# Kernel optimization log

Hardware: AMD Instinct MI355X
Metric: run time of the kernel (lower is better)

The kernel has to match this reference:

```python
import jax, jax.numpy as jnp
import numpy as np

EPS = 1e-08
ORDINAL = 2.0

def setup_inputs() -> dict:
    key = jax.random.key(0)
    k1, k2, k3, k4, k5 = jax.random.split(key, 5)
    B, IN, OUT = 1024, 256, 1024
    inputs = jax.random.normal(k1, (B, IN), dtype=jnp.float32)
    weights = jax.random.normal(k2, (OUT, IN), dtype=jnp.float32) * (1.0 / np.sqrt(IN))
    biases = jax.random.normal(k3, (OUT,), dtype=jnp.float32) * (1.0 / np.sqrt(IN))
    centers = jax.random.normal(k4, (OUT, IN), dtype=jnp.float32) * 0.1
    # diag inv covars ~ U(3/(IN+0.5), 3/(IN-0.5)) per reset_parameters
    inv_covars = jax.random.uniform(k5, (OUT, IN), dtype=jnp.float32,
                                    minval=3.0 / (IN + 0.5), maxval=3.0 / (IN - 0.5))
    return {"inputs": inputs, "weights": weights, "biases": biases,
            "centers": centers, "inv_covars": inv_covars}

def reference(inputs, weights, biases, centers, inv_covars):
    # linear part: [B, OUT]
    l = inputs @ weights.T + biases
    # diag covar path (ordinal = 2.0, so the 1e-32 stabilizer is absent and
    # pow(c^2, 1/ordinal) == |c| after clamping):
    # g[b, z] = sum_i ( |x[b,i] - c[z,i]| * sqrt(clamp(ic[z,i])^2) )^2
    ic = jnp.minimum(inv_covars, 1.0 / EPS)
    scale = jnp.power(ic * ic, 1.0 / ORDINAL)  # [OUT, IN]
    diff = jnp.abs(inputs[:, None, :] - centers[None, :, :]) * scale[None, :, :]  # [B, OUT, IN]
    g = jnp.exp(-jnp.sum(jnp.power(diff, ORDINAL), axis=-1))  # [B, OUT]
    res = l * g
    return (res, g)
```

## Files before the change

### kernel.cpp

```cpp
#include <hip/hip_runtime.h>
#include <math.h>


typedef __attribute__((ext_vector_type(8))) short short8;
typedef __attribute__((ext_vector_type(4))) float floatx4;

#define BDIM   1024
#define INDIM  256
#define OUTDIM 1024
#define AK     512
#define WK     256
#define GK     512

__device__ __forceinline__ unsigned short f2bf(float f) {
    union { float f; unsigned u; } v; v.f = f;
    unsigned r = v.u + 0x7FFFu + ((v.u >> 16) & 1u);
    return (unsigned short)(r >> 16);
}

__global__ __launch_bounds__(256)
void fgn_prep(const float* __restrict__ X, const float* __restrict__ W,
              const float* __restrict__ C, const float* __restrict__ IC,
              unsigned short* __restrict__ Ap, unsigned short* __restrict__ Wb,
              unsigned short* __restrict__ Gw, float* __restrict__ Cz)
{
    const int bid = blockIdx.x;
    if (bid < 256) {
        const int f   = bid * 256 + threadIdx.x;
        const int row = f >> 6;
        const int kq  = (f & 63) << 2;
        float4 x = *(const float4*)&X[row * INDIM + kq];
        ushort4 a, b;
        a.x = f2bf(x.x);      a.y = f2bf(x.y);      a.z = f2bf(x.z);      a.w = f2bf(x.w);
        b.x = f2bf(x.x*x.x);  b.y = f2bf(x.y*x.y);  b.z = f2bf(x.z*x.z);  b.w = f2bf(x.w*x.w);
        *(ushort4*)&Ap[row * AK + kq]         = a;
        *(ushort4*)&Ap[row * AK + INDIM + kq] = b;
    } else {
        const int z    = (bid - 256) * 4 + (threadIdx.x >> 6);
        const int lane = threadIdx.x & 63;
        const int k    = lane << 2;
        float4 w  = *(const float4*)&W [z * INDIM + k];
        float4 c  = *(const float4*)&C [z * INDIM + k];
        float4 ic = *(const float4*)&IC[z * INDIM + k];
        float s0 = fminf(ic.x, 1e8f), s1 = fminf(ic.y, 1e8f);
        float s2 = fminf(ic.z, 1e8f), s3 = fminf(ic.w, 1e8f);
        float q0 = s0*s0, q1 = s1*s1, q2 = s2*s2, q3 = s3*s3;
        ushort4 wv, w2v, s2v;
        wv.x  = f2bf(w.x);            wv.y  = f2bf(w.y);
        wv.z  = f2bf(w.z);            wv.w  = f2bf(w.w);
        w2v.x = f2bf(-2.f*c.x*q0);    w2v.y = f2bf(-2.f*c.y*q1);
        w2v.z = f2bf(-2.f*c.z*q2);    w2v.w = f2bf(-2.f*c.w*q3);
        s2v.x = f2bf(q0);             s2v.y = f2bf(q1);
        s2v.z = f2bf(q2);             s2v.w = f2bf(q3);
        *(ushort4*)&Wb[z * WK + k]         = wv;
        *(ushort4*)&Gw[z * GK + k]         = w2v;
        *(ushort4*)&Gw[z * GK + INDIM + k] = s2v;
        float cc = c.x*c.x*q0 + c.y*c.y*q1 + c.z*c.z*q2 + c.w*c.w*q3;
        #pragma unroll
        for (int off = 32; off; off >>= 1) cc += __shfl_xor(cc, off);
        if (lane == 0) Cz[z] = cc;
    }
}

__global__ __launch_bounds__(256)
void fgn_main(const unsigned short* __restrict__ Ap, const unsigned short* __restrict__ Wb,
              const unsigned short* __restrict__ Gw, const float* __restrict__ Bias,
              const float* __restrict__ Cz, float* __restrict__ Out)
{
    const int n0   = blockIdx.x * 32;
    const int m0   = blockIdx.y * 32;
    const int t    = threadIdx.x;
    const int w    = t >> 6;
    const int lane = t & 63;
    const int r    = lane & 15;
    const int q    = lane >> 4;

    __shared__ float sL[2 * 64 * 17];
    __shared__ float sG[4 * 64 * 17];

    const int kb = w * 16;
    const short8* A0 = (const short8*)(Ap + (size_t)(m0 +      r) * AK) + q + kb;
    const short8* A1 = (const short8*)(Ap + (size_t)(m0 + 16 + r) * AK) + q + kb;
    const short8* G0 = (const short8*)(Gw + (size_t)(n0 +      r) * GK) + q + kb;
    const short8* G1 = (const short8*)(Gw + (size_t)(n0 + 16 + r) * GK) + q + kb;
    const short8* W0 = (const short8*)(Wb + (size_t)(n0 +      r) * WK) + q + kb;
    const short8* W1 = (const short8*)(Wb + (size_t)(n0 + 16 + r) * WK) + q + kb;

    floatx4 zero = {0.f, 0.f, 0.f, 0.f};
    floatx4 accL[2][2] = {{zero, zero}, {zero, zero}};
    floatx4 accG[2][2] = {{zero, zero}, {zero, zero}};

    #pragma unroll
    for (int kk = 0; kk < 4; ++kk) {
        short8 a0 = A0[kk * 4];
        short8 a1 = A1[kk * 4];
        short8 g0 = G0[kk * 4];
        short8 g1 = G1[kk * 4];
        accG[0][0] = __builtin_amdgcn_mfma_f32_16x16x32_bf16(a0, g0, accG[0][0], 0, 0, 0);
        accG[0][1] = __builtin_amdgcn_mfma_f32_16x16x32_bf16(a0, g1, accG[0][1], 0, 0, 0);
        accG[1][0] = __builtin_amdgcn_mfma_f32_16x16x32_bf16(a1, g0, accG[1][0], 0, 0, 0);
        accG[1][1] = __builtin_amdgcn_mfma_f32_16x16x32_bf16(a1, g1, accG[1][1], 0, 0, 0);
        if (w < 2) {
            short8 w0 = W0[kk * 4];
            short8 w1 = W1[kk * 4];
            accL[0][0] = __builtin_amdgcn_mfma_f32_16x16x32_bf16(a0, w0, accL[0][0], 0, 0, 0);
            accL[0][1] = __builtin_amdgcn_mfma_f32_16x16x32_bf16(a0, w1, accL[0][1], 0, 0, 0);
            accL[1][0] = __builtin_amdgcn_mfma_f32_16x16x32_bf16(a1, w0, accL[1][0], 0, 0, 0);
            accL[1][1] = __builtin_amdgcn_mfma_f32_16x16x32_bf16(a1, w1, accL[1][1], 0, 0, 0);
        }
    }

    #pragma unroll
    for (int mt = 0; mt < 2; ++mt)
        #pragma unroll
        for (int nt = 0; nt < 2; ++nt)
            #pragma unroll
            for (int reg = 0; reg < 4; ++reg) {
                const int f = mt * 8 + nt * 4 + reg;
                sG[(w * 64 + lane) * 17 + f] = accG[mt][nt][reg];
                if (w < 2) sL[(w * 64 + lane) * 17 + f] = accL[mt][nt][reg];
            }
    __syncthreads();

    const int l  = lane;
    const int gr = w;
    const int li = l & 15;
    const float bias0 = Bias[n0 + li],  bias1 = Bias[n0 + 16 + li];
    const float cz0   = Cz[n0 + li],    cz1   = Cz[n0 + 16 + li];
    float* OutR = Out;
    float* OutG = Out + (size_t)BDIM * OUTDIM;
    #pragma unroll
    for (int j = 0; j < 4; ++j) {
        const int f = gr * 4 + j;
        const float Ls = sL[l * 17 + f] + sL[(64 + l) * 17 + f];
        const float Gs = sG[l * 17 + f]         + sG[(64 + l) * 17 + f]
                       + sG[(128 + l) * 17 + f] + sG[(192 + l) * 17 + f];
        const int mt = f >> 3, nt = (f >> 2) & 1, reg = f & 3;
        const int m = m0 + mt * 16 + (l >> 4) * 4 + reg;
        const int n = n0 + nt * 16 + li;
        const float g   = expf(-(Gs + (nt ? cz1 : cz0)));
        const float res = (Ls + (nt ? bias1 : bias0)) * g;
        OutR[(size_t)m * OUTDIM + n] = res;
        OutG[(size_t)m * OUTDIM + n] = g;
    }
}

extern "C" void kernel_launch(void* const* d_in, const int* in_sizes, int n_in,
                              void* d_out, int out_size, void* d_ws, size_t ws_size,
                              hipStream_t stream) {
    const float* X    = (const float*)d_in[0];
    const float* W    = (const float*)d_in[1];
    const float* Bias = (const float*)d_in[2];
    const float* C    = (const float*)d_in[3];
    const float* IC   = (const float*)d_in[4];
    float* Out = (float*)d_out;

    unsigned short* Ap = (unsigned short*)d_ws;
    unsigned short* Wb = Ap + (size_t)BDIM * AK;
    unsigned short* Gw = Wb + (size_t)OUTDIM * WK;
    float*          Cz = (float*)(Gw + (size_t)OUTDIM * GK);

    fgn_prep<<<512, 256, 0, stream>>>(X, W, C, IC, Ap, Wb, Gw, Cz);
    dim3 grid(OUTDIM / 32, BDIM / 32);
    fgn_main<<<grid, 256, 0, stream>>>(Ap, Wb, Gw, Bias, Cz, Out);
}
```

Measured before the change: 77.49 us.

## Fuse bf16 preprocessing into main GEMM kernel, dropping the prep launch

Removes the separate prep kernel and its bf16 workspace, so the main kernel reads fp32 X, W, C and IC directly and converts them to bf16 in registers. The c^2*q term is computed per tile with an extra MFMA against a vector of ones, and the K split now spreads the linear GEMM across all four waves. This saves a kernel launch and the workspace write and re-read, but every tile now reloads fp32 data at twice the bytes and repeats the conversion work, which 32x32 tiles re-read many times.

```diff
diff --git a/kernel.cpp b/kernel.cpp
--- a/kernel.cpp
+++ b/kernel.cpp
@@ -8,9 +8,6 @@
 #define BDIM   1024
 #define INDIM  256
 #define OUTDIM 1024
-#define AK     512
-#define WK     256
-#define GK     512
 
 __device__ __forceinline__ unsigned short f2bf(float f) {
     union { float f; unsigned u; } v; v.f = f;
@@ -18,54 +15,26 @@
     return (unsigned short)(r >> 16);
 }
 
-__global__ __launch_bounds__(256)
-void fgn_prep(const float* __restrict__ X, const float* __restrict__ W,
-              const float* __restrict__ C, const float* __restrict__ IC,
-              unsigned short* __restrict__ Ap, unsigned short* __restrict__ Wb,
-              unsigned short* __restrict__ Gw, float* __restrict__ Cz)
-{
-    const int bid = blockIdx.x;
-    if (bid < 256) {
-        const int f   = bid * 256 + threadIdx.x;
-        const int row = f >> 6;
-        const int kq  = (f & 63) << 2;
-        float4 x = *(const float4*)&X[row * INDIM + kq];
-        ushort4 a, b;
-        a.x = f2bf(x.x);      a.y = f2bf(x.y);      a.z = f2bf(x.z);      a.w = f2bf(x.w);
-        b.x = f2bf(x.x*x.x);  b.y = f2bf(x.y*x.y);  b.z = f2bf(x.z*x.z);  b.w = f2bf(x.w*x.w);
-        *(ushort4*)&Ap[row * AK + kq]         = a;
-        *(ushort4*)&Ap[row * AK + INDIM + kq] = b;
-    } else {
-        const int z    = (bid - 256) * 4 + (threadIdx.x >> 6);
-        const int lane = threadIdx.x & 63;
-        const int k    = lane << 2;
-        float4 w  = *(const float4*)&W [z * INDIM + k];
-        float4 c  = *(const float4*)&C [z * INDIM + k];
-        float4 ic = *(const float4*)&IC[z * INDIM + k];
-        float s0 = fminf(ic.x, 1e8f), s1 = fminf(ic.y, 1e8f);
-        float s2 = fminf(ic.z, 1e8f), s3 = fminf(ic.w, 1e8f);
-        float q0 = s0*s0, q1 = s1*s1, q2 = s2*s2, q3 = s3*s3;
-        ushort4 wv, w2v, s2v;
-        wv.x  = f2bf(w.x);            wv.y  = f2bf(w.y);
-        wv.z  = f2bf(w.z);            wv.w  = f2bf(w.w);
-        w2v.x = f2bf(-2.f*c.x*q0);    w2v.y = f2bf(-2.f*c.y*q1);
-        w2v.z = f2bf(-2.f*c.z*q2);    w2v.w = f2bf(-2.f*c.w*q3);
-        s2v.x = f2bf(q0);             s2v.y = f2bf(q1);
-        s2v.z = f2bf(q2);             s2v.w = f2bf(q3);
-        *(ushort4*)&Wb[z * WK + k]         = wv;
-        *(ushort4*)&Gw[z * GK + k]         = w2v;
-        *(ushort4*)&Gw[z * GK + INDIM + k] = s2v;
-        float cc = c.x*c.x*q0 + c.y*c.y*q1 + c.z*c.z*q2 + c.w*c.w*q3;
-        #pragma unroll
-        for (int off = 32; off; off >>= 1) cc += __shfl_xor(cc, off);
-        if (lane == 0) Cz[z] = cc;
-    }
+__device__ __forceinline__ void load8(const float* __restrict__ p, float f[8]) {
+    float4 v0 = *(const float4*)p;
+    float4 v1 = *(const float4*)(p + 4);
+    f[0]=v0.x; f[1]=v0.y; f[2]=v0.z; f[3]=v0.w;
+    f[4]=v1.x; f[5]=v1.y; f[6]=v1.z; f[7]=v1.w;
 }
 
+__device__ __forceinline__ short8 pack8(const float f[8]) {
+    short8 r;
+    #pragma unroll
+    for (int i = 0; i < 8; ++i) r[i] = (short)f2bf(f[i]);
+    return r;
+}
+
+#define MFMA __builtin_amdgcn_mfma_f32_16x16x32_bf16
+
 __global__ __launch_bounds__(256)
-void fgn_main(const unsigned short* __restrict__ Ap, const unsigned short* __restrict__ Wb,
-              const unsigned short* __restrict__ Gw, const float* __restrict__ Bias,
-              const float* __restrict__ Cz, float* __restrict__ Out)
+void fgn_fused(const float* __restrict__ X, const float* __restrict__ W,
+               const float* __restrict__ Bias, const float* __restrict__ C,
+               const float* __restrict__ IC, float* __restrict__ Out)
 {
     const int n0   = blockIdx.x * 32;
     const int m0   = blockIdx.y * 32;
@@ -75,38 +44,55 @@
     const int r    = lane & 15;
     const int q    = lane >> 4;
 
-    __shared__ float sL[2 * 64 * 17];
+    __shared__ float sL[4 * 64 * 17];
     __shared__ float sG[4 * 64 * 17];
-
-    const int kb = w * 16;
-    const short8* A0 = (const short8*)(Ap + (size_t)(m0 +      r) * AK) + q + kb;
-    const short8* A1 = (const short8*)(Ap + (size_t)(m0 + 16 + r) * AK) + q + kb;
-    const short8* G0 = (const short8*)(Gw + (size_t)(n0 +      r) * GK) + q + kb;
-    const short8* G1 = (const short8*)(Gw + (size_t)(n0 + 16 + r) * GK) + q + kb;
-    const short8* W0 = (const short8*)(Wb + (size_t)(n0 +      r) * WK) + q + kb;
-    const short8* W1 = (const short8*)(Wb + (size_t)(n0 + 16 + r) * WK) + q + kb;
+    __shared__ float sC[4][32];
 
     floatx4 zero = {0.f, 0.f, 0.f, 0.f};
     floatx4 accL[2][2] = {{zero, zero}, {zero, zero}};
     floatx4 accG[2][2] = {{zero, zero}, {zero, zero}};
+    floatx4 accC[2]    = {zero, zero};
+
+    short8 ones;
+    #pragma unroll
+    for (int i = 0; i < 8; ++i) ones[i] = (short)0x3F80;
 
     #pragma unroll
-    for (int kk = 0; kk < 4; ++kk) {
-        short8 a0 = A0[kk * 4];
-        short8 a1 = A1[kk * 4];
-        short8 g0 = G0[kk * 4];
-        short8 g1 = G1[kk * 4];
-        accG[0][0] = __builtin_amdgcn_mfma_f32_16x16x32_bf16(a0, g0, accG[0][0], 0, 0, 0);
-        accG[0][1] = __builtin_amdgcn_mfma_f32_16x16x32_bf16(a0, g1, accG[0][1], 0, 0, 0);
-        accG[1][0] = __builtin_amdgcn_mfma_f32_16x16x32_bf16(a1, g0, accG[1][0], 0, 0, 0);
-        accG[1][1] = __builtin_amdgcn_mfma_f32_16x16x32_bf16(a1, g1, accG[1][1], 0, 0, 0);
-        if (w < 2) {
-            short8 w0 = W0[kk * 4];
-            short8 w1 = W1[kk * 4];
-            accL[0][0] = __builtin_amdgcn_mfma_f32_16x16x32_bf16(a0, w0, accL[0][0], 0, 0, 0);
-            accL[0][1] = __builtin_amdgcn_mfma_f32_16x16x32_bf16(a0, w1, accL[0][1], 0, 0, 0);
-            accL[1][0] = __builtin_amdgcn_mfma_f32_16x16x32_bf16(a1, w0, accL[1][0], 0, 0, 0);
-            accL[1][1] = __builtin_amdgcn_mfma_f32_16x16x32_bf16(a1, w1, accL[1][1], 0, 0, 0);
+    for (int kk = 0; kk < 2; ++kk) {
+        const int k = w * 64 + kk * 32 + q * 8;
+        short8 a0[2], a2[2];
+        #pragma unroll
+        for (int mt = 0; mt < 2; ++mt) {
+            float x[8], xs[8];
+            load8(&X[(size_t)(m0 + mt * 16 + r) * INDIM + k], x);
+            #pragma unroll
+            for (int i = 0; i < 8; ++i) xs[i] = x[i] * x[i];
+            a0[mt] = pack8(x);
+            a2[mt] = pack8(xs);
+        }
+        #pragma unroll
+        for (int nt = 0; nt < 2; ++nt) {
+            const size_t ro = (size_t)(n0 + nt * 16 + r) * INDIM + k;
+            float wv[8], cv[8], iv[8], g1[8], g2[8], g3[8];
+            load8(&W[ro],  wv);
+            load8(&C[ro],  cv);
+            load8(&IC[ro], iv);
+            #pragma unroll
+            for (int i = 0; i < 8; ++i) {
+                float s  = fminf(iv[i], 1e8f);
+                float qq = s * s;
+                g2[i] = qq;
+                g1[i] = -2.f * cv[i] * qq;
+                g3[i] = cv[i] * cv[i] * qq;
+            }
+            short8 wf = pack8(wv), f1 = pack8(g1), f2 = pack8(g2), f3 = pack8(g3);
+            accL[0][nt] = MFMA(a0[0], wf, accL[0][nt], 0, 0, 0);
+            accL[1][nt] = MFMA(a0[1], wf, accL[1][nt], 0, 0, 0);
+            accG[0][nt] = MFMA(a0[0], f1, accG[0][nt], 0, 0, 0);
+            accG[1][nt] = MFMA(a0[1], f1, accG[1][nt], 0, 0, 0);
+            accG[0][nt] = MFMA(a2[0], f2, accG[0][nt], 0, 0, 0);
+            accG[1][nt] = MFMA(a2[1], f2, accG[1][nt], 0, 0, 0);
+            accC[nt]    = MFMA(ones,  f3, accC[nt],    0, 0, 0);
         }
     }
 
@@ -118,23 +104,31 @@
             for (int reg = 0; reg < 4; ++reg) {
                 const int f = mt * 8 + nt * 4 + reg;
                 sG[(w * 64 + lane) * 17 + f] = accG[mt][nt][reg];
-                if (w < 2) sL[(w * 64 + lane) * 17 + f] = accL[mt][nt][reg];
+                sL[(w * 64 + lane) * 17 + f] = accL[mt][nt][reg];
             }
+    if (q == 0) {
+        sC[w][r]      = accC[0][0];
+        sC[w][16 + r] = accC[1][0];
+    }
     __syncthreads();
 
     const int l  = lane;
-    const int gr = w;
     const int li = l & 15;
-    const float bias0 = Bias[n0 + li],  bias1 = Bias[n0 + 16 + li];
-    const float cz0   = Cz[n0 + li],    cz1   = Cz[n0 + 16 + li];
+    float cz0 = 0.f, cz1 = 0.f;
+    #pragma unroll
+    for (int ww = 0; ww < 4; ++ww) { cz0 += sC[ww][li]; cz1 += sC[ww][16 + li]; }
+    const float bias0 = Bias[n0 + li], bias1 = Bias[n0 + 16 + li];
     float* OutR = Out;
     float* OutG = Out + (size_t)BDIM * OUTDIM;
     #pragma unroll
     for (int j = 0; j < 4; ++j) {
-        const int f = gr * 4 + j;
-        const float Ls = sL[l * 17 + f] + sL[(64 + l) * 17 + f];
-        const float Gs = sG[l * 17 + f]         + sG[(64 + l) * 17 + f]
-                       + sG[(128 + l) * 17 + f] + sG[(192 + l) * 17 + f];
+        const int f = w * 4 + j;
+        float Ls = 0.f, Gs = 0.f;
+        #pragma unroll
+        for (int ww = 0; ww < 4; ++ww) {
+            Ls += sL[(ww * 64 + l) * 17 + f];
+            Gs += sG[(ww * 64 + l) * 17 + f];
+        }
         const int mt = f >> 3, nt = (f >> 2) & 1, reg = f & 3;
         const int m = m0 + mt * 16 + (l >> 4) * 4 + reg;
         const int n = n0 + nt * 16 + li;
@@ -155,12 +149,6 @@
     const float* IC   = (const float*)d_in[4];
     float* Out = (float*)d_out;
 
-    unsigned short* Ap = (unsigned short*)d_ws;
-    unsigned short* Wb = Ap + (size_t)BDIM * AK;
-    unsigned short* Gw = Wb + (size_t)OUTDIM * WK;
-    float*          Cz = (float*)(Gw + (size_t)OUTDIM * GK);
-
-    fgn_prep<<<512, 256, 0, stream>>>(X, W, C, IC, Ap, Wb, Gw, Cz);
     dim3 grid(OUTDIM / 32, BDIM / 32);
-    fgn_main<<<grid, 256, 0, stream>>>(Ap, Wb, Gw, Bias, Cz, Out);
+    fgn_fused<<<grid, 256, 0, stream>>>(X, W, Bias, C, IC, Out);
 }
```

Result: slower. 79.22 us (+2.2%).
